# Kernel tuning notes

Measured on AMD Instinct MI355X. Metric: run time of the kernel, lower is better.

## Reference

```python
import jax, jax.numpy as jnp
import numpy as np

B, H, W, C = 4, 128, 128, 256
D_MODEL, NH = 512, 8
DH = D_MODEL // NH  # 64


def setup_inputs() -> dict:
    key = jax.random.key(0)
    ks = jax.random.split(key, 5)
    s = lambda fan_in: 1.0 / np.sqrt(fan_in)
    return {
        "x": jax.random.normal(ks[0], (B, H, W, C), jnp.float32),
        "Wq": jax.random.normal(ks[1], (C, D_MODEL), jnp.float32) * s(C),
        "bq": jnp.zeros((D_MODEL,), jnp.float32),
        "Wk": jax.random.normal(ks[2], (C, D_MODEL), jnp.float32) * s(C),
        "bk": jnp.zeros((D_MODEL,), jnp.float32),
        "Wv": jax.random.normal(ks[3], (C, D_MODEL), jnp.float32) * s(C),
        "bv": jnp.zeros((D_MODEL,), jnp.float32),
        "Wo": jax.random.normal(ks[4], (D_MODEL, C), jnp.float32) * s(D_MODEL),
        "bo": jnp.zeros((C,), jnp.float32),
    }


def reference(x, Wq, bq, Wk, bk, Wv, bv, Wo, bo):
    # Axial multi-head attention along axis 1 (H), W axis is batched.
    b, h, w, _ = x.shape
    q = (x @ Wq + bq).reshape(b, h, w, NH, DH) * (DH ** -0.5)
    k = (x @ Wk + bk).reshape(b, h, w, NH, DH)
    v = (x @ Wv + bv).reshape(b, h, w, NH, DH)
    # scores over the H axis: [B, Nh, W, H, H]
    scores = jnp.einsum("bxwnd,bywnd->bnwxy", q, k)
    probs = jax.nn.softmax(scores, axis=-1)
    # [B, H, W, Nh, DH] -> [B, H, W, d_model]
    out = jnp.einsum("bnwxy,bywnd->bxwnd", probs, v).reshape(b, h, w, D_MODEL)
    # Wo projection; original combines to [B,W,H,C] then permutes back to [B,H,W,C],
    # which is equivalent to applying Wo directly here. Dropout is identity at inference.
    return out @ Wo + bo
```

## Files before the change

### kernel.cpp

```cpp
#include <hip/hip_runtime.h>

typedef unsigned short u16;
typedef __attribute__((ext_vector_type(8))) short bf16x8;
typedef __attribute__((ext_vector_type(8))) unsigned short u16x8;
typedef __attribute__((ext_vector_type(4))) float f32x4;

#define DEVI static __device__ __forceinline__

DEVI u16 f2b(float f) {
  unsigned u = __builtin_bit_cast(unsigned, f);
  return (u16)((u + 0x7FFFu + ((u >> 16) & 1u)) >> 16);
}

DEVI void gload_lds16(const void* g, void* l) {
  __builtin_amdgcn_global_load_lds(
      (const __attribute__((address_space(1))) unsigned int*)g,
      (__attribute__((address_space(3))) unsigned int*)l, 16, 0, 0);
}


__global__ __launch_bounds__(256) void prep_x(const float* __restrict__ x, u16* __restrict__ xb) {
  const int n8 = 65536 * 256 / 8;
  int i = blockIdx.x * blockDim.x + threadIdx.x;
  for (; i < n8; i += gridDim.x * blockDim.x) {
    const float4* p = (const float4*)x + (size_t)i * 2;
    float4 a = p[0], b = p[1];
    u16x8 r;
    r[0] = f2b(a.x); r[1] = f2b(a.y); r[2] = f2b(a.z); r[3] = f2b(a.w);
    r[4] = f2b(b.x); r[5] = f2b(b.y); r[6] = f2b(b.z); r[7] = f2b(b.w);
    *(u16x8*)(xb + (size_t)i * 8) = r;
  }
}

__global__ __launch_bounds__(256) void prep_w(
    const float* __restrict__ Wq, const float* __restrict__ Wk,
    const float* __restrict__ Wv, const float* __restrict__ Wo,
    const float* __restrict__ bq, const float* __restrict__ bk, const float* __restrict__ bv,
    u16* __restrict__ wqkvT, u16* __restrict__ woT, float* __restrict__ bqkv) {
  const int NW1 = 1536 * 256, NW2 = 256 * 512;
  const int total = NW1 + NW2 + 1536;
  int i = blockIdx.x * blockDim.x + threadIdx.x;
  for (; i < total; i += gridDim.x * blockDim.x) {
    if (i < NW1) {
      int nn = i >> 8, kk = i & 255;
      float v;
      if (nn < 512)       v = Wq[kk * 512 + nn] * 0.125f;
      else if (nn < 1024) v = Wk[kk * 512 + (nn - 512)];
      else                v = Wv[kk * 512 + (nn - 1024)];
      wqkvT[i] = f2b(v);
    } else if (i < NW1 + NW2) {
      int j = i - NW1;
      int nn = j >> 9, kk = j & 511;
      woT[j] = f2b(Wo[kk * 256 + nn]);
    } else {
      int j = i - NW1 - NW2;
      bqkv[j] = (j < 512) ? bq[j] * 0.125f : (j < 1024 ? bk[j - 512] : bv[j - 1024]);
    }
  }
}


template <int KK, bool OUT_BF16>
__global__ __launch_bounds__(1024) void gemm256(
    const u16* __restrict__ A, const u16* __restrict__ Bt,
    const float* __restrict__ bias, void* __restrict__ Cv, int N) {
  constexpr int NT = KK / 64;
  __shared__ u16 smem[65536];
  const int tid = threadIdx.x;
  const int lane = tid & 63, wid = tid >> 6;
  const int nTn = N >> 8;
  const int qx = gridDim.x >> 3;
  const int wg = (blockIdx.x & 7) * qx + (blockIdx.x >> 3);
  const long m0 = (long)(wg / nTn) * 256;
  const long n0 = (long)(wg % nTn) * 256;
  const int wr = wid >> 2, wc = wid & 3;
  const int hi = lane >> 4, lo = lane & 15;
  const u16* Ab = A + m0 * KK;
  const u16* Bb = Bt + n0 * KK;
  const int srow_ = tid >> 3;
  const int schunk = tid & 7;

  f32x4 acc[4][4];
#pragma unroll
  for (int mi = 0; mi < 4; ++mi)
#pragma unroll
    for (int ni = 0; ni < 4; ++ni) acc[mi][ni] = f32x4{0.f, 0.f, 0.f, 0.f};

  auto stage = [&](int t) {
    u16* base = &smem[(t & 1) * 32768];
    const int kt = t * 64;
#pragma unroll
    for (int j = 0; j < 2; ++j) {
      int row = j * 128 + srow_;
      int colE = (schunk ^ (row & 7)) << 3;
      gload_lds16(Ab + (long)row * KK + kt + colE, &base[(j * 1024 + tid) * 8]);
    }
#pragma unroll
    for (int j = 0; j < 2; ++j) {
      int row = j * 128 + srow_;
      int colE = (schunk ^ (row & 7)) << 3;
      gload_lds16(Bb + (long)row * KK + kt + colE, &base[16384 + (j * 1024 + tid) * 8]);
    }
  };

  stage(0);
#pragma unroll
  for (int t = 0; t < NT; ++t) {
    if (t + 1 < NT) {
      stage(t + 1);
      asm volatile("s_waitcnt vmcnt(4)" ::: "memory");
    } else {
      asm volatile("s_waitcnt vmcnt(0)" ::: "memory");
    }
    __builtin_amdgcn_sched_barrier(0);
    __builtin_amdgcn_s_barrier();
    const u16* aB = &smem[(t & 1) * 32768];
    const u16* bB = aB + 16384;
#pragma unroll
    for (int ks = 0; ks < 2; ++ks) {
      const int slot = ((hi + ks * 4) ^ (lo & 7)) << 3;
      bf16x8 af[4], bfr[4];
#pragma unroll
      for (int mi = 0; mi < 4; ++mi)
        af[mi] = *(const bf16x8*)&aB[(wr * 64 + mi * 16 + lo) * 64 + slot];
#pragma unroll
      for (int ni = 0; ni < 4; ++ni)
        bfr[ni] = *(const bf16x8*)&bB[(wc * 64 + ni * 16 + lo) * 64 + slot];
#pragma unroll
      for (int mi = 0; mi < 4; ++mi)
#pragma unroll
        for (int ni = 0; ni < 4; ++ni)
          acc[mi][ni] = __builtin_amdgcn_mfma_f32_16x16x32_bf16(af[mi], bfr[ni], acc[mi][ni], 0, 0, 0);
    }
    __builtin_amdgcn_sched_barrier(0);
    __builtin_amdgcn_s_barrier();
  }

  float bb[4];
#pragma unroll
  for (int ni = 0; ni < 4; ++ni) bb[ni] = bias[n0 + wc * 64 + ni * 16 + lo];

  if (OUT_BF16) {
    u16* Cg = (u16*)Cv;
#pragma unroll
    for (int mi = 0; mi < 4; ++mi)
#pragma unroll
      for (int ni = 0; ni < 4; ++ni) {
#pragma unroll
        for (int j = 0; j < 4; ++j) {
          int row = wr * 64 + mi * 16 + hi * 4 + j;
          int chunk = (wc * 8 + ni * 2 + (lo >> 3)) ^ ((row >> 2) & 7);
          smem[row * 256 + chunk * 8 + (lo & 7)] = f2b(acc[mi][ni][j] + bb[ni]);
        }
      }
    __syncthreads();
#pragma unroll
    for (int it = 0; it < 8; ++it) {
      int idx = it * 1024 + tid;
      int row = idx >> 5, c = idx & 31;
      int cs = c ^ ((row >> 2) & 7);
      *(u16x8*)(Cg + (m0 + row) * N + n0 + c * 8) = *(const u16x8*)&smem[row * 256 + cs * 8];
    }
  } else {
    float* Cg = (float*)Cv;
#pragma unroll
    for (int mi = 0; mi < 4; ++mi)
#pragma unroll
      for (int ni = 0; ni < 4; ++ni) {
        long cg = n0 + wc * 64 + ni * 16 + lo;
#pragma unroll
        for (int j = 0; j < 4; ++j)
          Cg[(m0 + wr * 64 + mi * 16 + hi * 4 + j) * N + cg] = acc[mi][ni][j] + bb[ni];
      }
  }
}


__global__ __launch_bounds__(256) void attn_axial(const u16* __restrict__ qkv,
                                                  u16* __restrict__ ao) {
  __shared__ u16 smem[24576];
  u16* kld = smem;
  u16* pld = smem;
  u16* vt  = smem + 16384;

  const int g = blockIdx.x;
  const int n = g & 7, w = (g >> 3) & 127, b = g >> 10;
  const int tid = threadIdx.x, lane = tid & 63, wid = tid >> 6;
  const size_t ystr = (size_t)128 * 1536;
  const size_t base = (size_t)(b * 16384 + w) * 1536;
  const size_t bq_ = base + n * 64;
  const size_t bk_ = base + 512 + n * 64;
  const size_t bv_ = base + 1024 + n * 64;
  const int hi = lane >> 4, lo = lane & 15;

  u16x8 kreg[4];
  const int kr0 = tid >> 3, kc = tid & 7;
#pragma unroll
  for (int i = 0; i < 4; ++i)
    kreg[i] = *(const u16x8*)(qkv + bk_ + (size_t)(i * 32 + kr0) * ystr + kc * 8);

  u16x8 va0, va1, vc0, vc1;
  const int vh2 = tid >> 6, vyp = (tid & 63) * 2;
  {
    const u16* g0 = qkv + bv_ + (size_t)vyp * ystr + vh2 * 16;
    va0 = *(const u16x8*)g0;
    va1 = *(const u16x8*)(g0 + 8);
    vc0 = *(const u16x8*)(g0 + ystr);
    vc1 = *(const u16x8*)(g0 + ystr + 8);
  }

  bf16x8 aq[2][2];
#pragma unroll
  for (int mi = 0; mi < 2; ++mi)
#pragma unroll
    for (int ks = 0; ks < 2; ++ks)
      aq[mi][ks] = *(const bf16x8*)(qkv + bq_ +
          (size_t)(wid * 32 + mi * 16 + lo) * ystr + hi * 8 + ks * 32);

#pragma unroll
  for (int i = 0; i < 4; ++i) {
    const int r = i * 32 + kr0;
    *(u16x8*)&kld[r * 64 + ((kc ^ (r & 7)) << 3)] = kreg[i];
  }
  {
    unsigned* vt32 = (unsigned*)vt;
    const int cch = vyp >> 3;
    const int cw = (vyp >> 1) & 3;
#pragma unroll
    for (int e = 0; e < 8; ++e) {
      const int d0 = vh2 * 16 + e, d1 = vh2 * 16 + 8 + e;
      const int c0s = (cch & 8) | ((cch & 7) ^ (d0 & 7));
      const int c1s = (cch & 8) | ((cch & 7) ^ (d1 & 7));
      vt32[d0 * 64 + c0s * 4 + cw] = (unsigned)va0[e] | ((unsigned)vc0[e] << 16);
      vt32[d1 * 64 + c1s * 4 + cw] = (unsigned)va1[e] | ((unsigned)vc1[e] << 16);
    }
  }
  __syncthreads();

  f32x4 s[2][8];
#pragma unroll
  for (int mi = 0; mi < 2; ++mi)
#pragma unroll
    for (int ni = 0; ni < 8; ++ni) s[mi][ni] = f32x4{0.f, 0.f, 0.f, 0.f};
  __builtin_amdgcn_s_setprio(1);
#pragma unroll
  for (int ks = 0; ks < 2; ++ks) {
#pragma unroll
    for (int ni = 0; ni < 8; ++ni) {
      const int kr = ni * 16 + lo;
      bf16x8 kf = *(const bf16x8*)&kld[kr * 64 + (((hi + ks * 4) ^ (kr & 7)) << 3)];
#pragma unroll
      for (int mi = 0; mi < 2; ++mi)
        s[mi][ni] = __builtin_amdgcn_mfma_f32_16x16x32_bf16(aq[mi][ks], kf, s[mi][ni], 0, 0, 0);
    }
  }
  __builtin_amdgcn_s_setprio(0);
  __syncthreads();

  float rinv[2][4];
#pragma unroll
  for (int mi = 0; mi < 2; ++mi) {
#pragma unroll
    for (int j = 0; j < 4; ++j) {
      float m = s[mi][0][j];
#pragma unroll
      for (int ni = 1; ni < 8; ++ni) m = fmaxf(m, s[mi][ni][j]);
#pragma unroll
      for (int d = 1; d < 16; d <<= 1) m = fmaxf(m, __shfl_xor(m, d, 64));
      float sum = 0.f;
#pragma unroll
      for (int ni = 0; ni < 8; ++ni) {
        float e = exp2f((s[mi][ni][j] - m) * 1.44269504f);
        s[mi][ni][j] = e;
        sum += e;
      }
#pragma unroll
      for (int d = 1; d < 16; d <<= 1) sum += __shfl_xor(sum, d, 64);
      rinv[mi][j] = 1.f / sum;
      const int q = wid * 32 + mi * 16 + hi * 4 + j;
#pragma unroll
      for (int ni = 0; ni < 8; ++ni) {
        const int yp = ni * 16 + lo;
        const int cch = yp >> 3;
        const int cs = (cch & 8) | ((cch & 7) ^ (q & 7));
        pld[q * 128 + cs * 8 + (yp & 7)] = f2b(s[mi][ni][j]);
      }
    }
  }

  f32x4 o[2][4];
#pragma unroll
  for (int mi = 0; mi < 2; ++mi)
#pragma unroll
    for (int ni = 0; ni < 4; ++ni) o[mi][ni] = f32x4{0.f, 0.f, 0.f, 0.f};
  __builtin_amdgcn_s_setprio(1);
#pragma unroll
  for (int ks = 0; ks < 4; ++ks) {
    const int cch = hi + ks * 4;
    bf16x8 ap[2];
#pragma unroll
    for (int mi = 0; mi < 2; ++mi) {
      const int pr = wid * 32 + mi * 16 + lo;
      const int cs = (cch & 8) | ((cch & 7) ^ (pr & 7));
      ap[mi] = *(const bf16x8*)&pld[pr * 128 + cs * 8];
    }
#pragma unroll
    for (int ni = 0; ni < 4; ++ni) {
      const int vr = ni * 16 + lo;
      const int cs = (cch & 8) | ((cch & 7) ^ (vr & 7));
      bf16x8 vf = *(const bf16x8*)&vt[vr * 128 + cs * 8];
#pragma unroll
      for (int mi = 0; mi < 2; ++mi)
        o[mi][ni] = __builtin_amdgcn_mfma_f32_16x16x32_bf16(ap[mi], vf, o[mi][ni], 0, 0, 0);
    }
  }
  __builtin_amdgcn_s_setprio(0);

#pragma unroll
  for (int mi = 0; mi < 2; ++mi)
#pragma unroll
    for (int j = 0; j < 4; ++j) {
      const int q = wid * 32 + mi * 16 + hi * 4 + j;
      const size_t obase = ((size_t)(b * 16384 + q * 128 + w)) * 512 + (size_t)n * 64;
#pragma unroll
      for (int ni = 0; ni < 4; ++ni)
        ao[obase + ni * 16 + lo] = f2b(o[mi][ni][j] * rinv[mi][j]);
    }
}


extern "C" void kernel_launch(void* const* d_in, const int* in_sizes, int n_in,
                              void* d_out, int out_size, void* d_ws, size_t ws_size,
                              hipStream_t stream) {
  (void)in_sizes; (void)n_in; (void)out_size; (void)ws_size;
  const float* x  = (const float*)d_in[0];
  const float* Wq = (const float*)d_in[1];
  const float* bq = (const float*)d_in[2];
  const float* Wk = (const float*)d_in[3];
  const float* bk = (const float*)d_in[4];
  const float* Wv = (const float*)d_in[5];
  const float* bv = (const float*)d_in[6];
  const float* Wo = (const float*)d_in[7];
  const float* bo = (const float*)d_in[8];
  float* out = (float*)d_out;

  char* ws = (char*)d_ws;
  const size_t MiB = (size_t)1 << 20;
  u16* qkv   = (u16*)ws;
  u16* xb    = (u16*)(ws + 192 * MiB);
  u16* wqkvT = (u16*)(ws + 224 * MiB);
  u16* woT   = wqkvT + 1536 * 256;
  float* bqkv = (float*)(woT + 256 * 512);

  prep_x<<<2048, 256, 0, stream>>>(x, xb);
  prep_w<<<512, 256, 0, stream>>>(Wq, Wk, Wv, Wo, bq, bk, bv, wqkvT, woT, bqkv);

  gemm256<256, true><<<1536, 1024, 0, stream>>>(xb, wqkvT, bqkv, qkv, 1536);
  attn_axial<<<4096, 256, 0, stream>>>(qkv, (u16*)out);
  gemm256<512, false><<<256, 1024, 0, stream>>>((const u16*)out, woT, bo, out, 256);
}
```

Measured before the change: 225.9 us.

## Keep softmax probabilities in registers via transposed QK^T and lane shuffles

The attention kernel now computes S^T (K as the A operand, Q as B), so each query's scores sit in one lane column and the softmax reduction needs only two cross-lane shuffles. Normalized probabilities are packed to bf16 with v_cvt_pk_bf16_f32 and rearranged into MFMA A-operand layout through xor shuffles, replacing the LDS round trip for P. K is read directly from global memory instead of being staged in LDS, which shrinks shared memory to the V tile only, and launch bounds now request 4 blocks per SM. This removes one barrier and the LDS traffic for K and P. In exchange it adds shuffle and register pressure and uncoalesced global K loads, and it rounds normalized P to bf16 rather than applying the normalization afterward.

```diff
diff --git a/kernel.cpp b/kernel.cpp
--- a/kernel.cpp
+++ b/kernel.cpp
@@ -3,6 +3,7 @@
 typedef unsigned short u16;
 typedef __attribute__((ext_vector_type(8))) short bf16x8;
 typedef __attribute__((ext_vector_type(8))) unsigned short u16x8;
+typedef __attribute__((ext_vector_type(4))) unsigned u32x4;
 typedef __attribute__((ext_vector_type(4))) float f32x4;
 
 #define DEVI static __device__ __forceinline__
@@ -10,6 +11,12 @@
 DEVI u16 f2b(float f) {
   unsigned u = __builtin_bit_cast(unsigned, f);
   return (u16)((u + 0x7FFFu + ((u >> 16) & 1u)) >> 16);
+}
+
+DEVI unsigned cvtpk(float a, float b) {
+  unsigned r;
+  asm("v_cvt_pk_bf16_f32 %0, %1, %2" : "=v"(r) : "v"(a), "v"(b));
+  return r;
 }
 
 DEVI void gload_lds16(const void* g, void* l) {
@@ -176,12 +183,9 @@
 }
 
 
-__global__ __launch_bounds__(256) void attn_axial(const u16* __restrict__ qkv,
-                                                  u16* __restrict__ ao) {
-  __shared__ u16 smem[24576];
-  u16* kld = smem;
-  u16* pld = smem;
-  u16* vt  = smem + 16384;
+__global__ __launch_bounds__(256, 4) void attn_axial(const u16* __restrict__ qkv,
+                                                     u16* __restrict__ ao) {
+  __shared__ u16 vt[8192];
 
   const int g = blockIdx.x;
   const int n = g & 7, w = (g >> 3) & 127, b = g >> 10;
@@ -193,138 +197,150 @@
   const size_t bv_ = base + 1024 + n * 64;
   const int hi = lane >> 4, lo = lane & 15;
 
-  u16x8 kreg[4];
-  const int kr0 = tid >> 3, kc = tid & 7;
-#pragma unroll
-  for (int i = 0; i < 4; ++i)
-    kreg[i] = *(const u16x8*)(qkv + bk_ + (size_t)(i * 32 + kr0) * ystr + kc * 8);
-
-  u16x8 va0, va1, vc0, vc1;
-  const int vh2 = tid >> 6, vyp = (tid & 63) * 2;
-  {
-    const u16* g0 = qkv + bv_ + (size_t)vyp * ystr + vh2 * 16;
-    va0 = *(const u16x8*)g0;
-    va1 = *(const u16x8*)(g0 + 8);
-    vc0 = *(const u16x8*)(g0 + ystr);
-    vc1 = *(const u16x8*)(g0 + ystr + 8);
-  }
-
-  bf16x8 aq[2][2];
-#pragma unroll
-  for (int mi = 0; mi < 2; ++mi)
+  const int vyp = (tid & 63) * 2;
+  const u16* vg = qkv + bv_ + (size_t)vyp * ystr + wid * 16;
+  u16x8 va0 = *(const u16x8*)vg;
+  u16x8 va1 = *(const u16x8*)(vg + 8);
+  u16x8 vc0 = *(const u16x8*)(vg + ystr);
+  u16x8 vc1 = *(const u16x8*)(vg + ystr + 8);
+
+  bf16x8 qf[2][2];
+#pragma unroll
+  for (int cg = 0; cg < 2; ++cg)
 #pragma unroll
     for (int ks = 0; ks < 2; ++ks)
-      aq[mi][ks] = *(const bf16x8*)(qkv + bq_ +
-          (size_t)(wid * 32 + mi * 16 + lo) * ystr + hi * 8 + ks * 32);
-
-#pragma unroll
-  for (int i = 0; i < 4; ++i) {
-    const int r = i * 32 + kr0;
-    *(u16x8*)&kld[r * 64 + ((kc ^ (r & 7)) << 3)] = kreg[i];
-  }
+      qf[cg][ks] = *(const bf16x8*)(qkv + bq_ +
+          (size_t)(wid * 32 + cg * 16 + lo) * ystr + hi * 8 + ks * 32);
+
+  f32x4 s2[2][8];
+#pragma unroll
+  for (int cg = 0; cg < 2; ++cg)
+#pragma unroll
+    for (int ni = 0; ni < 8; ++ni) s2[cg][ni] = f32x4{0.f, 0.f, 0.f, 0.f};
+  __builtin_amdgcn_s_setprio(1);
+#pragma unroll
+  for (int ks = 0; ks < 2; ++ks)
+#pragma unroll
+    for (int ni = 0; ni < 8; ++ni) {
+      bf16x8 kf = *(const bf16x8*)(qkv + bk_ +
+          (size_t)(ni * 16 + lo) * ystr + hi * 8 + ks * 32);
+      s2[0][ni] = __builtin_amdgcn_mfma_f32_16x16x32_bf16(kf, qf[0][ks], s2[0][ni], 0, 0, 0);
+      s2[1][ni] = __builtin_amdgcn_mfma_f32_16x16x32_bf16(kf, qf[1][ks], s2[1][ni], 0, 0, 0);
+    }
+  __builtin_amdgcn_s_setprio(0);
+
   {
     unsigned* vt32 = (unsigned*)vt;
     const int cch = vyp >> 3;
     const int cw = (vyp >> 1) & 3;
 #pragma unroll
     for (int e = 0; e < 8; ++e) {
-      const int d0 = vh2 * 16 + e, d1 = vh2 * 16 + 8 + e;
+      const int d0 = wid * 16 + e, d1 = wid * 16 + 8 + e;
       const int c0s = (cch & 8) | ((cch & 7) ^ (d0 & 7));
       const int c1s = (cch & 8) | ((cch & 7) ^ (d1 & 7));
       vt32[d0 * 64 + c0s * 4 + cw] = (unsigned)va0[e] | ((unsigned)vc0[e] << 16);
       vt32[d1 * 64 + c1s * 4 + cw] = (unsigned)va1[e] | ((unsigned)vc1[e] << 16);
     }
   }
+
+  unsigned setA[2][4][2], setB[2][4][2];
+#pragma unroll
+  for (int cg = 0; cg < 2; ++cg) {
+    float mx = s2[cg][0][0];
+#pragma unroll
+    for (int ni = 0; ni < 8; ++ni)
+#pragma unroll
+      for (int j = 0; j < 4; ++j) mx = fmaxf(mx, s2[cg][ni][j]);
+    mx = fmaxf(mx, __shfl_xor(mx, 16, 64));
+    mx = fmaxf(mx, __shfl_xor(mx, 32, 64));
+    float sum = 0.f;
+#pragma unroll
+    for (int ni = 0; ni < 8; ++ni)
+#pragma unroll
+      for (int j = 0; j < 4; ++j) {
+        float e = exp2f((s2[cg][ni][j] - mx) * 1.44269504f);
+        s2[cg][ni][j] = e;
+        sum += e;
+      }
+    sum += __shfl_xor(sum, 16, 64);
+    sum += __shfl_xor(sum, 32, 64);
+    const float r = 1.f / sum;
+
+    unsigned pkE[4][2], pkO[4][2];
+#pragma unroll
+    for (int o = 0; o < 4; ++o) {
+      pkE[o][0] = cvtpk(s2[cg][2 * o][0] * r, s2[cg][2 * o][1] * r);
+      pkE[o][1] = cvtpk(s2[cg][2 * o][2] * r, s2[cg][2 * o][3] * r);
+      pkO[o][0] = cvtpk(s2[cg][2 * o + 1][0] * r, s2[cg][2 * o + 1][1] * r);
+      pkO[o][1] = cvtpk(s2[cg][2 * o + 1][2] * r, s2[cg][2 * o + 1][3] * r);
+    }
+    const bool lowHi = (hi < 2);
+    unsigned keepR[4][2], gotR[4][2];
+#pragma unroll
+    for (int o = 0; o < 4; ++o)
+#pragma unroll
+      for (int e = 0; e < 2; ++e) {
+        unsigned snd = lowHi ? pkO[o][e] : pkE[o][e];
+        keepR[o][e] = lowHi ? pkE[o][e] : pkO[o][e];
+        gotR[o][e] = __shfl_xor(snd, 32, 64);
+      }
+    const bool fwdGot = (hi == 0) || (hi == 3);
+    unsigned recv2[4][2];
+#pragma unroll
+    for (int o = 0; o < 4; ++o)
+#pragma unroll
+      for (int e = 0; e < 2; ++e) {
+        unsigned snd = fwdGot ? gotR[o][e] : keepR[o][e];
+        recv2[o][e] = __shfl_xor(snd, 16, 64);
+      }
+#pragma unroll
+    for (int o = 0; o < 4; ++o)
+#pragma unroll
+      for (int e = 0; e < 2; ++e) {
+        setA[cg][o][e] = (hi & 1) ? recv2[o][e] : (hi == 0 ? keepR[o][e] : gotR[o][e]);
+        setB[cg][o][e] = (hi & 1) ? (hi == 1 ? gotR[o][e] : keepR[o][e]) : recv2[o][e];
+      }
+  }
+
   __syncthreads();
 
-  f32x4 s[2][8];
-#pragma unroll
-  for (int mi = 0; mi < 2; ++mi)
-#pragma unroll
-    for (int ni = 0; ni < 8; ++ni) s[mi][ni] = f32x4{0.f, 0.f, 0.f, 0.f};
-  __builtin_amdgcn_s_setprio(1);
-#pragma unroll
-  for (int ks = 0; ks < 2; ++ks) {
-#pragma unroll
-    for (int ni = 0; ni < 8; ++ni) {
-      const int kr = ni * 16 + lo;
-      bf16x8 kf = *(const bf16x8*)&kld[kr * 64 + (((hi + ks * 4) ^ (kr & 7)) << 3)];
-#pragma unroll
-      for (int mi = 0; mi < 2; ++mi)
-        s[mi][ni] = __builtin_amdgcn_mfma_f32_16x16x32_bf16(aq[mi][ks], kf, s[mi][ni], 0, 0, 0);
-    }
-  }
-  __builtin_amdgcn_s_setprio(0);
-  __syncthreads();
-
-  float rinv[2][4];
-#pragma unroll
-  for (int mi = 0; mi < 2; ++mi) {
-#pragma unroll
-    for (int j = 0; j < 4; ++j) {
-      float m = s[mi][0][j];
-#pragma unroll
-      for (int ni = 1; ni < 8; ++ni) m = fmaxf(m, s[mi][ni][j]);
-#pragma unroll
-      for (int d = 1; d < 16; d <<= 1) m = fmaxf(m, __shfl_xor(m, d, 64));
-      float sum = 0.f;
-#pragma unroll
-      for (int ni = 0; ni < 8; ++ni) {
-        float e = exp2f((s[mi][ni][j] - m) * 1.44269504f);
-        s[mi][ni][j] = e;
-        sum += e;
-      }
-#pragma unroll
-      for (int d = 1; d < 16; d <<= 1) sum += __shfl_xor(sum, d, 64);
-      rinv[mi][j] = 1.f / sum;
-      const int q = wid * 32 + mi * 16 + hi * 4 + j;
-#pragma unroll
-      for (int ni = 0; ni < 8; ++ni) {
-        const int yp = ni * 16 + lo;
-        const int cch = yp >> 3;
-        const int cs = (cch & 8) | ((cch & 7) ^ (q & 7));
-        pld[q * 128 + cs * 8 + (yp & 7)] = f2b(s[mi][ni][j]);
-      }
-    }
-  }
-
-  f32x4 o[2][4];
-#pragma unroll
-  for (int mi = 0; mi < 2; ++mi)
-#pragma unroll
-    for (int ni = 0; ni < 4; ++ni) o[mi][ni] = f32x4{0.f, 0.f, 0.f, 0.f};
+  f32x4 o2[2][4];
+#pragma unroll
+  for (int cg = 0; cg < 2; ++cg)
+#pragma unroll
+    for (int ni = 0; ni < 4; ++ni) o2[cg][ni] = f32x4{0.f, 0.f, 0.f, 0.f};
   __builtin_amdgcn_s_setprio(1);
 #pragma unroll
   for (int ks = 0; ks < 4; ++ks) {
     const int cch = hi + ks * 4;
-    bf16x8 ap[2];
-#pragma unroll
-    for (int mi = 0; mi < 2; ++mi) {
-      const int pr = wid * 32 + mi * 16 + lo;
-      const int cs = (cch & 8) | ((cch & 7) ^ (pr & 7));
-      ap[mi] = *(const bf16x8*)&pld[pr * 128 + cs * 8];
+    bf16x8 pa[2];
+#pragma unroll
+    for (int cg = 0; cg < 2; ++cg) {
+      u32x4 t;
+      t[0] = setA[cg][ks][0]; t[1] = setA[cg][ks][1];
+      t[2] = setB[cg][ks][0]; t[3] = setB[cg][ks][1];
+      pa[cg] = __builtin_bit_cast(bf16x8, t);
     }
 #pragma unroll
     for (int ni = 0; ni < 4; ++ni) {
       const int vr = ni * 16 + lo;
       const int cs = (cch & 8) | ((cch & 7) ^ (vr & 7));
       bf16x8 vf = *(const bf16x8*)&vt[vr * 128 + cs * 8];
-#pragma unroll
-      for (int mi = 0; mi < 2; ++mi)
-        o[mi][ni] = __builtin_amdgcn_mfma_f32_16x16x32_bf16(ap[mi], vf, o[mi][ni], 0, 0, 0);
+      o2[0][ni] = __builtin_amdgcn_mfma_f32_16x16x32_bf16(pa[0], vf, o2[0][ni], 0, 0, 0);
+      o2[1][ni] = __builtin_amdgcn_mfma_f32_16x16x32_bf16(pa[1], vf, o2[1][ni], 0, 0, 0);
     }
   }
   __builtin_amdgcn_s_setprio(0);
 
 #pragma unroll
-  for (int mi = 0; mi < 2; ++mi)
+  for (int cg = 0; cg < 2; ++cg)
 #pragma unroll
     for (int j = 0; j < 4; ++j) {
-      const int q = wid * 32 + mi * 16 + hi * 4 + j;
+      const int q = wid * 32 + cg * 16 + hi * 4 + j;
       const size_t obase = ((size_t)(b * 16384 + q * 128 + w)) * 512 + (size_t)n * 64;
 #pragma unroll
       for (int ni = 0; ni < 4; ++ni)
-        ao[obase + ni * 16 + lo] = f2b(o[mi][ni][j] * rinv[mi][j]);
+        ao[obase + ni * 16 + lo] = f2b(o2[cg][ni][j]);
     }
 }
 
```

Measured after the change: 244.8 us. +8.4%, slower.
